# Optimization experiments

Measured on AMD Instinct MI355X. Metric: run time of the kernel, lower is better.

Reference implementation:

```python
import jax, jax.numpy as jnp
import numpy as np

BN_EPS = 1e-5
CLUSTER_SIZE = 32  # K (real clusters kept after softmax)


def setup_inputs() -> dict:
    key = jax.random.key(0)
    ks = jax.random.split(key, 7)
    B, N, D, Ktot, K = 4096, 128, 512, 48, 32
    x = jax.random.normal(ks[0], (B, N, D), dtype=jnp.float32)
    clusters = jax.random.normal(ks[1], (D, Ktot), dtype=jnp.float32) / np.sqrt(D)
    bn_w = jax.random.uniform(ks[2], (Ktot,), dtype=jnp.float32)
    bn_b = jax.random.normal(ks[3], (Ktot,), dtype=jnp.float32)
    bn_rm = jax.random.normal(ks[4], (Ktot,), dtype=jnp.float32)
    bn_rv = jax.random.uniform(ks[5], (Ktot,), dtype=jnp.float32)  # positive variance
    clusters2 = jax.random.normal(ks[6], (1, D, K), dtype=jnp.float32) / np.sqrt(D)
    return {"x": x, "clusters": clusters, "bn_w": bn_w, "bn_b": bn_b,
            "bn_rm": bn_rm, "bn_rv": bn_rv, "clusters2": clusters2}


def reference(x, clusters, bn_w, bn_b, bn_rm, bn_rv, clusters2):
    # x: [B, N, D]; clusters: [D, Ktot]; clusters2: [1, D, K]
    B, N, D = x.shape
    K = clusters2.shape[-1]
    # cluster projection: [B, N, Ktot]
    logits = jnp.einsum('bnd,dk->bnk', x, clusters)
    # inference BatchNorm1d (affine with running stats)
    inv_std = jax.lax.rsqrt(bn_rv + BN_EPS)
    logits = (logits - bn_rm) * inv_std * bn_w + bn_b
    # softmax over real + ghost clusters, then drop ghost (no renorm)
    assignment = jax.nn.softmax(logits, axis=-1)[..., :K]  # [B, N, K]
    a_sum = jnp.sum(assignment, axis=1, keepdims=True)      # [B, 1, K]
    a = a_sum * clusters2                                   # [B, D, K]
    # weighted VLAD accumulate: [B, D, K]
    vlad = jnp.einsum('bnk,bnd->bdk', assignment, x) - a
    # intra-normalize (L2 across descriptor dim D, per cluster)
    vlad = vlad / jnp.maximum(jnp.linalg.norm(vlad, axis=1, keepdims=True), 1e-12)
    # flatten and L2-normalize full vector
    vlad = vlad.reshape(B, D * K)
    vlad = vlad / jnp.maximum(jnp.linalg.norm(vlad, axis=1, keepdims=True), 1e-12)
    return vlad
```

## Files before the change

kernel.cpp:

```cpp
#include <hip/hip_runtime.h>

typedef unsigned short u16;
typedef __attribute__((ext_vector_type(8))) short short8;
typedef __attribute__((ext_vector_type(4))) float f32x4;
typedef __attribute__((ext_vector_type(4))) u16 u16x4;

#define NPT 128
#define DIM 512
#define KT 48
#define KC 32

__device__ __forceinline__ u16 f2bf(float f) {
    unsigned u = __builtin_bit_cast(unsigned, f);
    return (u16)((u + 0x7FFFu + ((u >> 16) & 1u)) >> 16);
}

__global__ void prep_kernel(const float* __restrict__ clusters,
                            const float* __restrict__ bn_w,
                            const float* __restrict__ bn_b,
                            const float* __restrict__ bn_rm,
                            const float* __restrict__ bn_rv,
                            u16* __restrict__ cTs,
                            float* __restrict__ tvec) {
    const int k = blockIdx.x;
    const float s = bn_w[k] * rsqrtf(bn_rv[k] + 1e-5f);
    if (threadIdx.x == 0) tvec[k] = bn_b[k] - bn_rm[k] * s;
    for (int d = threadIdx.x; d < DIM; d += blockDim.x)
        cTs[k * DIM + d] = f2bf(clusters[d * KT + k] * s);
}

__global__ __launch_bounds__(512)
void vlad_kernel(const float* __restrict__ x,
                 const float* __restrict__ c2,
                 const u16* __restrict__ cTs,
                 const float* __restrict__ tvec,
                 float* __restrict__ out) {
    __shared__ __align__(16) u16 xs[NPT * DIM];
    __shared__ __align__(16) u16 aT[KC][136];
    __shared__ float t_s[KT];
    __shared__ float asum_part[8][KC];
    __shared__ float asum_s[KC];
    __shared__ float colsq_part[8][KC];
    __shared__ float scalek[KC];

    const int b    = blockIdx.x;
    const int tid  = threadIdx.x;
    const int wave = tid >> 6;
    const int lane = tid & 63;
    const int lr   = lane & 15;
    const int lg   = lane >> 4;

    if (tid < KT) t_s[tid] = tvec[tid];

    {
        const f32x4* gx = (const f32x4*)(x + (size_t)b * (NPT * DIM));
        #pragma unroll 4
        for (int it = 0; it < 32; ++it) {
            int c = tid + it * 512;
            f32x4 v = gx[c];
            int n  = c >> 7;
            int d0 = (c & 127) << 2;
            u16x4 w;
            w[0] = f2bf(v[0]); w[1] = f2bf(v[1]); w[2] = f2bf(v[2]); w[3] = f2bf(v[3]);
            int byteoff = n * 1024 + ((2 * d0) ^ ((n & 7) << 4));
            *(u16x4*)((char*)xs + byteoff) = w;
        }
    }
    __syncthreads();

    f32x4 acc0 = {0.f,0.f,0.f,0.f}, acc1 = {0.f,0.f,0.f,0.f}, acc2 = {0.f,0.f,0.f,0.f};
    {
        const int nrow = wave * 16 + lr;
        const int rowbase = nrow * 1024;
        const int sw = (nrow & 7) << 4;
        #pragma unroll 2
        for (int step = 0; step < 16; ++step) {
            const int d0 = step * 32 + lg * 8;
            short8 af = *(const short8*)((const char*)xs + (rowbase + ((2 * d0) ^ sw)));
            short8 b0 = *(const short8*)(cTs + (0 * 16 + lr) * DIM + d0);
            short8 b1 = *(const short8*)(cTs + (1 * 16 + lr) * DIM + d0);
            short8 b2 = *(const short8*)(cTs + (2 * 16 + lr) * DIM + d0);
            acc0 = __builtin_amdgcn_mfma_f32_16x16x32_bf16(af, b0, acc0, 0, 0, 0);
            acc1 = __builtin_amdgcn_mfma_f32_16x16x32_bf16(af, b1, acc1, 0, 0, 0);
            acc2 = __builtin_amdgcn_mfma_f32_16x16x32_bf16(af, b2, acc2, 0, 0, 0);
        }
    }
    {
        const float t0 = t_s[lr], t1 = t_s[16 + lr], t2 = t_s[32 + lr];
        float a0[4], a1[4];
        #pragma unroll
        for (int r = 0; r < 4; ++r) {
            float l0 = acc0[r] + t0, l1 = acc1[r] + t1, l2 = acc2[r] + t2;
            float m = fmaxf(fmaxf(l0, l1), l2);
            #pragma unroll
            for (int o = 1; o < 16; o <<= 1) m = fmaxf(m, __shfl_xor(m, o));
            float e0 = __expf(l0 - m), e1 = __expf(l1 - m), e2 = __expf(l2 - m);
            float s = e0 + e1 + e2;
            #pragma unroll
            for (int o = 1; o < 16; o <<= 1) s += __shfl_xor(s, o);
            float inv = 1.0f / s;
            a0[r] = e0 * inv; a1[r] = e1 * inv;
        }
        float p0 = 0.f, p1 = 0.f;
        #pragma unroll
        for (int r = 0; r < 4; ++r) {
            int n = wave * 16 + lg * 4 + r;
            aT[lr][n]      = f2bf(a0[r]);
            aT[16 + lr][n] = f2bf(a1[r]);
            p0 += a0[r]; p1 += a1[r];
        }
        p0 += __shfl_xor(p0, 16); p0 += __shfl_xor(p0, 32);
        p1 += __shfl_xor(p1, 16); p1 += __shfl_xor(p1, 32);
        if (lane < 16) { asum_part[wave][lane] = p0; asum_part[wave][16 + lane] = p1; }
    }
    __syncthreads();
    if (tid < KC) {
        float s = 0.f;
        #pragma unroll
        for (int w2 = 0; w2 < 8; ++w2) s += asum_part[w2][tid];
        asum_s[tid] = s;
    }

    f32x4 vacc[4][2];
    #pragma unroll
    for (int i = 0; i < 4; ++i) {
        vacc[i][0] = (f32x4){0.f,0.f,0.f,0.f};
        vacc[i][1] = (f32x4){0.f,0.f,0.f,0.f};
    }
    #pragma unroll
    for (int ns = 0; ns < 4; ++ns) {
        short8 b0 = *(const short8*)(&aT[lr][ns * 32 + lg * 8]);
        short8 b1 = *(const short8*)(&aT[16 + lr][ns * 32 + lg * 8]);
        #pragma unroll
        for (int dti = 0; dti < 4; ++dti) {
            const int d = (wave * 4 + dti) * 16 + lr;
            const int base = (ns * 32 + lg * 8) * 1024 + 2 * d;
            short8 af;
            #pragma unroll
            for (int j = 0; j < 8; ++j)
                af[j] = *(const short*)((const char*)xs + ((base + j * 1024) ^ (j << 4)));
            vacc[dti][0] = __builtin_amdgcn_mfma_f32_16x16x32_bf16(af, b0, vacc[dti][0], 0, 0, 0);
            vacc[dti][1] = __builtin_amdgcn_mfma_f32_16x16x32_bf16(af, b1, vacc[dti][1], 0, 0, 0);
        }
    }
    __syncthreads();

    float vv[4][2][4];
    float cs0 = 0.f, cs1 = 0.f;
    const float as0 = asum_s[lr], as1 = asum_s[16 + lr];
    #pragma unroll
    for (int dti = 0; dti < 4; ++dti) {
        #pragma unroll
        for (int r = 0; r < 4; ++r) {
            int d = (wave * 4 + dti) * 16 + lg * 4 + r;
            float v0 = vacc[dti][0][r] - as0 * c2[d * KC + lr];
            float v1 = vacc[dti][1][r] - as1 * c2[d * KC + 16 + lr];
            vv[dti][0][r] = v0; vv[dti][1][r] = v1;
            cs0 += v0 * v0; cs1 += v1 * v1;
        }
    }
    cs0 += __shfl_xor(cs0, 16); cs0 += __shfl_xor(cs0, 32);
    cs1 += __shfl_xor(cs1, 16); cs1 += __shfl_xor(cs1, 32);
    if (lane < 16) { colsq_part[wave][lane] = cs0; colsq_part[wave][16 + lane] = cs1; }
    __syncthreads();
    if (tid < KC) {
        float sq = 0.f;
        #pragma unroll
        for (int w2 = 0; w2 < 8; ++w2) sq += colsq_part[w2][tid];
        float cn = sqrtf(sq);
        float s1 = 1.0f / fmaxf(cn, 1e-12f);
        float c1 = cn * s1;
        float tot = c1 * c1;
        #pragma unroll
        for (int o = 1; o < 32; o <<= 1) tot += __shfl_xor(tot, o);
        scalek[tid] = s1 * (1.0f / fmaxf(sqrtf(tot), 1e-12f));
    }
    __syncthreads();
    {
        float* ob = out + (size_t)b * (DIM * KC);
        const float sk0 = scalek[lr], sk1 = scalek[16 + lr];
        #pragma unroll
        for (int dti = 0; dti < 4; ++dti) {
            #pragma unroll
            for (int r = 0; r < 4; ++r) {
                int d = (wave * 4 + dti) * 16 + lg * 4 + r;
                ob[d * KC + lr]      = vv[dti][0][r] * sk0;
                ob[d * KC + 16 + lr] = vv[dti][1][r] * sk1;
            }
        }
    }
}

extern "C" void kernel_launch(void* const* d_in, const int* in_sizes, int n_in,
                              void* d_out, int out_size, void* d_ws, size_t ws_size,
                              hipStream_t stream) {
    const float* x        = (const float*)d_in[0];
    const float* clusters = (const float*)d_in[1];
    const float* bn_w     = (const float*)d_in[2];
    const float* bn_b     = (const float*)d_in[3];
    const float* bn_rm    = (const float*)d_in[4];
    const float* bn_rv    = (const float*)d_in[5];
    const float* c2       = (const float*)d_in[6];
    float* out = (float*)d_out;

    u16*   cTs  = (u16*)d_ws;
    float* tvec = (float*)((char*)d_ws + KT * DIM * sizeof(u16));

    const int B = in_sizes[0] / (NPT * DIM);

    prep_kernel<<<KT, 256, 0, stream>>>(clusters, bn_w, bn_b, bn_rm, bn_rv, cTs, tvec);
    vlad_kernel<<<B, 512, 0, stream>>>(x, c2, cTs, tvec, out);
}
```

Before: 444.8 us.

## Chunk points into two LDS halves to fit two blocks per CU

Result: slower. 516.8 us (+16.2%).

```diff
diff --git a/kernel.cpp b/kernel.cpp
--- a/kernel.cpp
+++ b/kernel.cpp
@@ -9,6 +9,8 @@
 #define DIM 512
 #define KT 48
 #define KC 32
+#define CH 64
+#define NCHUNK 2
 
 __device__ __forceinline__ u16 f2bf(float f) {
     unsigned u = __builtin_bit_cast(unsigned, f);
@@ -29,18 +31,18 @@
         cTs[k * DIM + d] = f2bf(clusters[d * KT + k] * s);
 }
 
-__global__ __launch_bounds__(512)
+__global__ __launch_bounds__(256, 2)
 void vlad_kernel(const float* __restrict__ x,
                  const float* __restrict__ c2,
                  const u16* __restrict__ cTs,
                  const float* __restrict__ tvec,
                  float* __restrict__ out) {
-    __shared__ __align__(16) u16 xs[NPT * DIM];
-    __shared__ __align__(16) u16 aT[KC][136];
+    __shared__ __align__(16) u16 xs[CH * DIM];
+    __shared__ __align__(16) u16 aT[KC][72];
     __shared__ float t_s[KT];
-    __shared__ float asum_part[8][KC];
+    __shared__ float asum_part[4][KC];
     __shared__ float asum_s[KC];
-    __shared__ float colsq_part[8][KC];
+    __shared__ float colsq_part[4][KC];
     __shared__ float scalek[KC];
 
     const int b    = blockIdx.x;
@@ -52,111 +54,125 @@
 
     if (tid < KT) t_s[tid] = tvec[tid];
 
-    {
-        const f32x4* gx = (const f32x4*)(x + (size_t)b * (NPT * DIM));
-        #pragma unroll 4
-        for (int it = 0; it < 32; ++it) {
-            int c = tid + it * 512;
-            f32x4 v = gx[c];
-            int n  = c >> 7;
-            int d0 = (c & 127) << 2;
-            u16x4 w;
-            w[0] = f2bf(v[0]); w[1] = f2bf(v[1]); w[2] = f2bf(v[2]); w[3] = f2bf(v[3]);
-            int byteoff = n * 1024 + ((2 * d0) ^ ((n & 7) << 4));
-            *(u16x4*)((char*)xs + byteoff) = w;
-        }
-    }
-    __syncthreads();
-
-    f32x4 acc0 = {0.f,0.f,0.f,0.f}, acc1 = {0.f,0.f,0.f,0.f}, acc2 = {0.f,0.f,0.f,0.f};
-    {
-        const int nrow = wave * 16 + lr;
-        const int rowbase = nrow * 1024;
-        const int sw = (nrow & 7) << 4;
-        #pragma unroll 2
-        for (int step = 0; step < 16; ++step) {
-            const int d0 = step * 32 + lg * 8;
-            short8 af = *(const short8*)((const char*)xs + (rowbase + ((2 * d0) ^ sw)));
-            short8 b0 = *(const short8*)(cTs + (0 * 16 + lr) * DIM + d0);
-            short8 b1 = *(const short8*)(cTs + (1 * 16 + lr) * DIM + d0);
-            short8 b2 = *(const short8*)(cTs + (2 * 16 + lr) * DIM + d0);
-            acc0 = __builtin_amdgcn_mfma_f32_16x16x32_bf16(af, b0, acc0, 0, 0, 0);
-            acc1 = __builtin_amdgcn_mfma_f32_16x16x32_bf16(af, b1, acc1, 0, 0, 0);
-            acc2 = __builtin_amdgcn_mfma_f32_16x16x32_bf16(af, b2, acc2, 0, 0, 0);
-        }
-    }
-    {
-        const float t0 = t_s[lr], t1 = t_s[16 + lr], t2 = t_s[32 + lr];
-        float a0[4], a1[4];
-        #pragma unroll
-        for (int r = 0; r < 4; ++r) {
-            float l0 = acc0[r] + t0, l1 = acc1[r] + t1, l2 = acc2[r] + t2;
-            float m = fmaxf(fmaxf(l0, l1), l2);
-            #pragma unroll
-            for (int o = 1; o < 16; o <<= 1) m = fmaxf(m, __shfl_xor(m, o));
-            float e0 = __expf(l0 - m), e1 = __expf(l1 - m), e2 = __expf(l2 - m);
-            float s = e0 + e1 + e2;
-            #pragma unroll
-            for (int o = 1; o < 16; o <<= 1) s += __shfl_xor(s, o);
-            float inv = 1.0f / s;
-            a0[r] = e0 * inv; a1[r] = e1 * inv;
-        }
-        float p0 = 0.f, p1 = 0.f;
-        #pragma unroll
-        for (int r = 0; r < 4; ++r) {
-            int n = wave * 16 + lg * 4 + r;
-            aT[lr][n]      = f2bf(a0[r]);
-            aT[16 + lr][n] = f2bf(a1[r]);
-            p0 += a0[r]; p1 += a1[r];
-        }
-        p0 += __shfl_xor(p0, 16); p0 += __shfl_xor(p0, 32);
-        p1 += __shfl_xor(p1, 16); p1 += __shfl_xor(p1, 32);
-        if (lane < 16) { asum_part[wave][lane] = p0; asum_part[wave][16 + lane] = p1; }
-    }
-    __syncthreads();
-    if (tid < KC) {
-        float s = 0.f;
-        #pragma unroll
-        for (int w2 = 0; w2 < 8; ++w2) s += asum_part[w2][tid];
-        asum_s[tid] = s;
-    }
-
-    f32x4 vacc[4][2];
+    f32x4 vacc[8][2];
     #pragma unroll
-    for (int i = 0; i < 4; ++i) {
+    for (int i = 0; i < 8; ++i) {
         vacc[i][0] = (f32x4){0.f,0.f,0.f,0.f};
         vacc[i][1] = (f32x4){0.f,0.f,0.f,0.f};
     }
-    #pragma unroll
-    for (int ns = 0; ns < 4; ++ns) {
-        short8 b0 = *(const short8*)(&aT[lr][ns * 32 + lg * 8]);
-        short8 b1 = *(const short8*)(&aT[16 + lr][ns * 32 + lg * 8]);
-        #pragma unroll
-        for (int dti = 0; dti < 4; ++dti) {
-            const int d = (wave * 4 + dti) * 16 + lr;
-            const int base = (ns * 32 + lg * 8) * 1024 + 2 * d;
-            short8 af;
-            #pragma unroll
-            for (int j = 0; j < 8; ++j)
-                af[j] = *(const short*)((const char*)xs + ((base + j * 1024) ^ (j << 4)));
-            vacc[dti][0] = __builtin_amdgcn_mfma_f32_16x16x32_bf16(af, b0, vacc[dti][0], 0, 0, 0);
-            vacc[dti][1] = __builtin_amdgcn_mfma_f32_16x16x32_bf16(af, b1, vacc[dti][1], 0, 0, 0);
+
+    for (int c = 0; c < NCHUNK; ++c) {
+        __syncthreads();
+
+        {
+            const f32x4* gx = (const f32x4*)(x + (size_t)b * (NPT * DIM) + c * (CH * DIM));
+            #pragma unroll 8
+            for (int it = 0; it < 32; ++it) {
+                int ci = tid + it * 256;
+                f32x4 v = __builtin_nontemporal_load(&gx[ci]);
+                int n  = ci >> 7;
+                int d0 = (ci & 127) << 2;
+                u16x4 w;
+                w[0] = f2bf(v[0]); w[1] = f2bf(v[1]); w[2] = f2bf(v[2]); w[3] = f2bf(v[3]);
+                int byteoff = n * 1024 + ((2 * d0) ^ ((n & 7) << 4));
+                *(u16x4*)((char*)xs + byteoff) = w;
+            }
+        }
+        __syncthreads();
+
+        f32x4 acc0 = {0.f,0.f,0.f,0.f}, acc1 = {0.f,0.f,0.f,0.f}, acc2 = {0.f,0.f,0.f,0.f};
+        {
+            const int nrow = wave * 16 + lr;
+            const int rowbase = nrow * 1024;
+            const int sw = (nrow & 7) << 4;
+            #pragma unroll 4
+            for (int step = 0; step < 16; ++step) {
+                const int d0 = step * 32 + lg * 8;
+                short8 af = *(const short8*)((const char*)xs + (rowbase + ((2 * d0) ^ sw)));
+                short8 b0 = *(const short8*)(cTs + (0 * 16 + lr) * DIM + d0);
+                short8 b1 = *(const short8*)(cTs + (1 * 16 + lr) * DIM + d0);
+                short8 b2 = *(const short8*)(cTs + (2 * 16 + lr) * DIM + d0);
+                acc0 = __builtin_amdgcn_mfma_f32_16x16x32_bf16(af, b0, acc0, 0, 0, 0);
+                acc1 = __builtin_amdgcn_mfma_f32_16x16x32_bf16(af, b1, acc1, 0, 0, 0);
+                acc2 = __builtin_amdgcn_mfma_f32_16x16x32_bf16(af, b2, acc2, 0, 0, 0);
+            }
+        }
+        {
+            const float t0 = t_s[lr], t1 = t_s[16 + lr], t2 = t_s[32 + lr];
+            float a0[4], a1[4];
+            #pragma unroll
+            for (int r = 0; r < 4; ++r) {
+                float l0 = acc0[r] + t0, l1 = acc1[r] + t1, l2 = acc2[r] + t2;
+                float m = fmaxf(fmaxf(l0, l1), l2);
+                #pragma unroll
+                for (int o = 1; o < 16; o <<= 1) m = fmaxf(m, __shfl_xor(m, o));
+                float e0 = __expf(l0 - m), e1 = __expf(l1 - m), e2 = __expf(l2 - m);
+                float s = e0 + e1 + e2;
+                #pragma unroll
+                for (int o = 1; o < 16; o <<= 1) s += __shfl_xor(s, o);
+                float inv = 1.0f / s;
+                a0[r] = e0 * inv; a1[r] = e1 * inv;
+            }
+            float p0 = 0.f, p1 = 0.f;
+            #pragma unroll
+            for (int r = 0; r < 4; ++r) {
+                int n = wave * 16 + lg * 4 + r;
+                aT[lr][n]      = f2bf(a0[r]);
+                aT[16 + lr][n] = f2bf(a1[r]);
+                p0 += a0[r]; p1 += a1[r];
+            }
+            p0 += __shfl_xor(p0, 16); p0 += __shfl_xor(p0, 32);
+            p1 += __shfl_xor(p1, 16); p1 += __shfl_xor(p1, 32);
+            if (lane < 16) {
+                if (c == 0) {
+                    asum_part[wave][lane]      = p0;
+                    asum_part[wave][16 + lane] = p1;
+                } else {
+                    asum_part[wave][lane]      += p0;
+                    asum_part[wave][16 + lane] += p1;
+                }
+            }
+        }
+        __syncthreads();
+        if (c == NCHUNK - 1 && tid < KC) {
+            float s = 0.f;
+            #pragma unroll
+            for (int w2 = 0; w2 < 4; ++w2) s += asum_part[w2][tid];
+            asum_s[tid] = s;
+        }
+
+        #pragma unroll
+        for (int ns = 0; ns < 2; ++ns) {
+            short8 b0 = *(const short8*)(&aT[lr][ns * 32 + lg * 8]);
+            short8 b1 = *(const short8*)(&aT[16 + lr][ns * 32 + lg * 8]);
+            #pragma unroll
+            for (int dti = 0; dti < 8; ++dti) {
+                const int d = wave * 128 + dti * 16 + lr;
+                const int base = (ns * 32 + lg * 8) * 1024 + 2 * d;
+                short8 af;
+                #pragma unroll
+                for (int j = 0; j < 8; ++j)
+                    af[j] = *(const short*)((const char*)xs + ((base + j * 1024) ^ (j << 4)));
+                vacc[dti][0] = __builtin_amdgcn_mfma_f32_16x16x32_bf16(af, b0, vacc[dti][0], 0, 0, 0);
+                vacc[dti][1] = __builtin_amdgcn_mfma_f32_16x16x32_bf16(af, b1, vacc[dti][1], 0, 0, 0);
+            }
         }
     }
     __syncthreads();
 
-    float vv[4][2][4];
     float cs0 = 0.f, cs1 = 0.f;
-    const float as0 = asum_s[lr], as1 = asum_s[16 + lr];
-    #pragma unroll
-    for (int dti = 0; dti < 4; ++dti) {
-        #pragma unroll
-        for (int r = 0; r < 4; ++r) {
-            int d = (wave * 4 + dti) * 16 + lg * 4 + r;
-            float v0 = vacc[dti][0][r] - as0 * c2[d * KC + lr];
-            float v1 = vacc[dti][1][r] - as1 * c2[d * KC + 16 + lr];
-            vv[dti][0][r] = v0; vv[dti][1][r] = v1;
-            cs0 += v0 * v0; cs1 += v1 * v1;
+    {
+        const float as0 = asum_s[lr], as1 = asum_s[16 + lr];
+        #pragma unroll
+        for (int dti = 0; dti < 8; ++dti) {
+            #pragma unroll
+            for (int r = 0; r < 4; ++r) {
+                int d = wave * 128 + dti * 16 + lg * 4 + r;
+                float v0 = vacc[dti][0][r] - as0 * c2[d * KC + lr];
+                float v1 = vacc[dti][1][r] - as1 * c2[d * KC + 16 + lr];
+                vacc[dti][0][r] = v0; vacc[dti][1][r] = v1;
+                cs0 += v0 * v0; cs1 += v1 * v1;
+            }
         }
     }
     cs0 += __shfl_xor(cs0, 16); cs0 += __shfl_xor(cs0, 32);
@@ -166,7 +182,7 @@
     if (tid < KC) {
         float sq = 0.f;
         #pragma unroll
-        for (int w2 = 0; w2 < 8; ++w2) sq += colsq_part[w2][tid];
+        for (int w2 = 0; w2 < 4; ++w2) sq += colsq_part[w2][tid];
         float cn = sqrtf(sq);
         float s1 = 1.0f / fmaxf(cn, 1e-12f);
         float c1 = cn * s1;
@@ -180,12 +196,12 @@
         float* ob = out + (size_t)b * (DIM * KC);
         const float sk0 = scalek[lr], sk1 = scalek[16 + lr];
         #pragma unroll
-        for (int dti = 0; dti < 4; ++dti) {
-            #pragma unroll
-            for (int r = 0; r < 4; ++r) {
-                int d = (wave * 4 + dti) * 16 + lg * 4 + r;
-                ob[d * KC + lr]      = vv[dti][0][r] * sk0;
-                ob[d * KC + 16 + lr] = vv[dti][1][r] * sk1;
+        for (int dti = 0; dti < 8; ++dti) {
+            #pragma unroll
+            for (int r = 0; r < 4; ++r) {
+                int d = wave * 128 + dti * 16 + lg * 4 + r;
+                ob[d * KC + lr]      = vacc[dti][0][r] * sk0;
+                ob[d * KC + 16 + lr] = vacc[dti][1][r] * sk1;
             }
         }
     }
@@ -209,5 +225,5 @@
     const int B = in_sizes[0] / (NPT * DIM);
 
     prep_kernel<<<KT, 256, 0, stream>>>(clusters, bn_w, bn_b, bn_rm, bn_rv, cTs, tvec);
-    vlad_kernel<<<B, 512, 0, stream>>>(x, c2, cTs, tvec, out);
-}
+    vlad_kernel<<<B, 256, 0, stream>>>(x, c2, cTs, tvec, out);
+}
```

## Load x per-wave with packed bf16 conversion and drop the first barrier

Applied to the files above, without the earlier changes.

New measurement: 438.2 us. Within noise of the previous version (-1.5%).

```diff
diff --git a/kernel.cpp b/kernel.cpp
--- a/kernel.cpp
+++ b/kernel.cpp
@@ -1,9 +1,10 @@
 #include <hip/hip_runtime.h>
 
 typedef unsigned short u16;
+typedef unsigned int u32;
 typedef __attribute__((ext_vector_type(8))) short short8;
 typedef __attribute__((ext_vector_type(4))) float f32x4;
-typedef __attribute__((ext_vector_type(4))) u16 u16x4;
+typedef __attribute__((ext_vector_type(2))) u32 u32x2;
 
 #define NPT 128
 #define DIM 512
@@ -13,6 +14,16 @@
 __device__ __forceinline__ u16 f2bf(float f) {
     unsigned u = __builtin_bit_cast(unsigned, f);
     return (u16)((u + 0x7FFFu + ((u >> 16) & 1u)) >> 16);
+}
+
+__device__ __forceinline__ u32 cvtpk(float lo, float hi) {
+    u32 r;
+    asm("v_cvt_pk_bf16_f32 %0, %1, %2" : "=v"(r) : "v"(lo), "v"(hi));
+    return r;
+}
+
+__device__ __forceinline__ int swz(int n) {
+    return ((n & 7) ^ ((n >> 3) & 7)) << 4;
 }
 
 __global__ void prep_kernel(const float* __restrict__ clusters,
@@ -37,7 +48,6 @@
                  float* __restrict__ out) {
     __shared__ __align__(16) u16 xs[NPT * DIM];
     __shared__ __align__(16) u16 aT[KC][136];
-    __shared__ float t_s[KT];
     __shared__ float asum_part[8][KC];
     __shared__ float asum_s[KC];
     __shared__ float colsq_part[8][KC];
@@ -50,29 +60,34 @@
     const int lr   = lane & 15;
     const int lg   = lane >> 4;
 
-    if (tid < KT) t_s[tid] = tvec[tid];
-
-    {
-        const f32x4* gx = (const f32x4*)(x + (size_t)b * (NPT * DIM));
-        #pragma unroll 4
-        for (int it = 0; it < 32; ++it) {
-            int c = tid + it * 512;
-            f32x4 v = gx[c];
-            int n  = c >> 7;
-            int d0 = (c & 127) << 2;
-            u16x4 w;
-            w[0] = f2bf(v[0]); w[1] = f2bf(v[1]); w[2] = f2bf(v[2]); w[3] = f2bf(v[3]);
-            int byteoff = n * 1024 + ((2 * d0) ^ ((n & 7) << 4));
-            *(u16x4*)((char*)xs + byteoff) = w;
-        }
-    }
-    __syncthreads();
+    {
+        const float* gxw = x + (size_t)b * (NPT * DIM) + (wave * 16) * DIM;
+        #pragma unroll
+        for (int bt = 0; bt < 4; ++bt) {
+            f32x4 tmp[8];
+            #pragma unroll
+            for (int i = 0; i < 8; ++i) {
+                int it = bt * 8 + i;
+                tmp[i] = *(const f32x4*)(gxw + (it >> 1) * DIM + (it & 1) * 256 + lane * 4);
+            }
+            #pragma unroll
+            for (int i = 0; i < 8; ++i) {
+                int it = bt * 8 + i;
+                int r = wave * 16 + (it >> 1);
+                u32x2 w2;
+                w2[0] = cvtpk(tmp[i][0], tmp[i][1]);
+                w2[1] = cvtpk(tmp[i][2], tmp[i][3]);
+                int off = ((it & 1) * 512 + lane * 8) ^ swz(r);
+                *(u32x2*)((char*)xs + r * 1024 + off) = w2;
+            }
+        }
+    }
 
     f32x4 acc0 = {0.f,0.f,0.f,0.f}, acc1 = {0.f,0.f,0.f,0.f}, acc2 = {0.f,0.f,0.f,0.f};
     {
         const int nrow = wave * 16 + lr;
         const int rowbase = nrow * 1024;
-        const int sw = (nrow & 7) << 4;
+        const int sw = swz(nrow);
         #pragma unroll 2
         for (int step = 0; step < 16; ++step) {
             const int d0 = step * 32 + lg * 8;
@@ -86,7 +101,7 @@
         }
     }
     {
-        const float t0 = t_s[lr], t1 = t_s[16 + lr], t2 = t_s[32 + lr];
+        const float t0 = tvec[lr], t1 = tvec[16 + lr], t2 = tvec[32 + lr];
         float a0[4], a1[4];
         #pragma unroll
         for (int r = 0; r < 4; ++r) {
@@ -131,14 +146,17 @@
     for (int ns = 0; ns < 4; ++ns) {
         short8 b0 = *(const short8*)(&aT[lr][ns * 32 + lg * 8]);
         short8 b1 = *(const short8*)(&aT[16 + lr][ns * 32 + lg * 8]);
+        const int n0 = ns * 32 + lg * 8;
+        const int q  = (ns * 4 + lg) & 7;
+        const char* pbase = (const char*)xs + n0 * 1024;
         #pragma unroll
         for (int dti = 0; dti < 4; ++dti) {
             const int d = (wave * 4 + dti) * 16 + lr;
-            const int base = (ns * 32 + lg * 8) * 1024 + 2 * d;
+            const int twod = 2 * d;
             short8 af;
             #pragma unroll
             for (int j = 0; j < 8; ++j)
-                af[j] = *(const short*)((const char*)xs + ((base + j * 1024) ^ (j << 4)));
+                af[j] = *(const short*)(pbase + j * 1024 + (twod ^ ((j ^ q) << 4)));
             vacc[dti][0] = __builtin_amdgcn_mfma_f32_16x16x32_bf16(af, b0, vacc[dti][0], 0, 0, 0);
             vacc[dti][1] = __builtin_amdgcn_mfma_f32_16x16x32_bf16(af, b1, vacc[dti][1], 0, 0, 0);
         }
```
